# Kernel tuning notes

Measured on AMD Instinct MI355X. Metric: run time of the kernel, lower is better.

## Reference

```python
import jax, jax.numpy as jnp
import numpy as np

ROI_SIZES = (3, 7, 11)
IMAGE_SIZE = 960.0


def setup_inputs() -> dict:
    key = jax.random.key(0)
    ks = jax.random.split(key, 12)
    B, C, H, W = 1, 64, 120, 120
    N = 4096
    feature_maps = jax.random.normal(ks[0], (B, C, H, W), jnp.float32)
    cx = jax.random.uniform(ks[1], (N,), jnp.float32, 100.0, 860.0)
    cy = jax.random.uniform(ks[2], (N,), jnp.float32, 100.0, 860.0)
    bw = jax.random.uniform(ks[3], (N,), jnp.float32, 20.0, 240.0)
    bh = jax.random.uniform(ks[4], (N,), jnp.float32, 20.0, 240.0)
    boxes = jnp.stack([cx - bw / 2, cy - bh / 2, cx + bw / 2, cy + bh / 2], axis=1)
    s = 0.05
    w1 = jax.random.normal(ks[5], (64, 128), jnp.float32) * s
    b1 = jnp.zeros((128,), jnp.float32)
    w2 = jax.random.normal(ks[6], (128, 64), jnp.float32) * s
    b2 = jnp.zeros((64,), jnp.float32)
    p1 = jax.random.normal(ks[7], (256, 128), jnp.float32) * s
    pb1 = jnp.zeros((128,), jnp.float32)
    p2 = jax.random.normal(ks[8], (128, 64), jnp.float32) * s
    pb2 = jnp.zeros((64,), jnp.float32)
    return dict(feature_maps=feature_maps, boxes=boxes, w1=w1, b1=b1, w2=w2, b2=b2,
                p1=p1, pb1=pb1, p2=p2, pb2=pb2)


def _roi_pool(fm0, boxes_norm, r):
    """affine_grid + bilinear grid_sample (align_corners=False, zeros pad) + global avg pool.
    fm0: [C,H,W], boxes_norm: [N,4] in [-1,1]. Returns [N,C]."""
    C, H, W = fm0.shape
    x1, y1, x2, y2 = boxes_norm[:, 0], boxes_norm[:, 1], boxes_norm[:, 2], boxes_norm[:, 3]
    cx = (x1 + x2) / 2
    cy = (y1 + y2) / 2
    bw = jnp.clip(x2 - x1, 1e-6, None)
    bh = jnp.clip(y2 - y1, 1e-6, None)
    # affine_grid base coords with align_corners=False: (2i+1)/r - 1
    lin = (2.0 * jnp.arange(r, dtype=jnp.float32) + 1.0) / r - 1.0
    gx = cx[:, None, None] + (bw / 2)[:, None, None] * lin[None, None, :]  # [N,r,r]
    gy = cy[:, None, None] + (bh / 2)[:, None, None] * lin[None, :, None]  # [N,r,r]
    # normalized -> pixel coords (align_corners=False)
    ix = ((gx + 1.0) * W - 1.0) / 2.0
    iy = ((gy + 1.0) * H - 1.0) / 2.0
    x0f = jnp.floor(ix)
    y0f = jnp.floor(iy)
    wx1 = ix - x0f
    wy1 = iy - y0f
    x0 = x0f.astype(jnp.int32)
    y0 = y0f.astype(jnp.int32)
    fm_flat = fm0.reshape(C, H * W)

    def corner(xi, yi, wt):
        valid = (xi >= 0) & (xi < W) & (yi >= 0) & (yi < H)
        xi_c = jnp.clip(xi, 0, W - 1)
        yi_c = jnp.clip(yi, 0, H - 1)
        idx = yi_c * W + xi_c  # [N,r,r]
        vals = jnp.take(fm_flat, idx.reshape(-1), axis=1).reshape(C, *idx.shape)  # [C,N,r,r]
        return vals * (wt * valid.astype(wt.dtype))[None]

    out = (corner(x0, y0, (1 - wx1) * (1 - wy1))
           + corner(x0 + 1, y0, wx1 * (1 - wy1))
           + corner(x0, y0 + 1, (1 - wx1) * wy1)
           + corner(x0 + 1, y0 + 1, wx1 * wy1))
    return out.mean(axis=(2, 3)).T  # [N,C]


def _shared_head(x, w1, b1, w2, b2):
    h = jax.nn.relu(x @ w1 + b1)
    return jax.nn.relu(h @ w2 + b2)


def reference(feature_maps, boxes, w1, b1, w2, b2, p1, pb1, p2, pb2):
    B, C, H, W = feature_maps.shape
    N = boxes.shape[0]
    boxes_norm = boxes / IMAGE_SIZE * 2.0 - 1.0
    fm0 = feature_maps[0]
    feats = []
    for r in ROI_SIZES:
        pooled = _roi_pool(fm0, boxes_norm, r)  # [N,C]
        feats.append(_shared_head(pooled, w1, b1, w2, b2))
    # global context: avg-pool full map, expand to N
    g = feature_maps.mean(axis=(2, 3))  # [B,C], B=1
    g = jnp.broadcast_to(g, (N, C))
    feats.append(_shared_head(g, w1, b1, w2, b2))
    concat = jnp.concatenate(feats, axis=1)  # [N, 4*64]
    h = jax.nn.relu(concat @ p1 + pb1)
    return jax.nn.relu(h @ p2 + pb2)
```

## Files before the change

kernel.cpp:

```cpp
#include <hip/hip_runtime.h>
#include <hip/hip_bf16.h>


#define HW 120
#define NPIX (HW * HW)

__device__ __forceinline__ float rdlane(float v, int l) {
    return __int_as_float(__builtin_amdgcn_readlane(__float_as_int(v), l));
}

__global__ __launch_bounds__(256) void k_transpose_mean(
    const float* __restrict__ fm, float* __restrict__ fm_t,
    float* __restrict__ partial)
{
    __shared__ float tile[64][65];
    __shared__ float pr[4][64];
    const int t  = threadIdx.x;
    const int tx = t & 63;
    const int ty = t >> 6;
    const int pix0 = blockIdx.x * 64;

    #pragma unroll
    for (int k = 0; k < 16; ++k) {
        const int c = k * 4 + ty;
        tile[c][tx] = fm[c * NPIX + pix0 + tx];
    }
    __syncthreads();
    #pragma unroll
    for (int k = 0; k < 16; ++k) {
        const int p = k * 4 + ty;
        fm_t[(pix0 + p) * 64 + tx] = tile[tx][p];
    }
    float s = 0.f;
    #pragma unroll
    for (int k = 0; k < 16; ++k) s += tile[tx][ty * 16 + k];
    pr[ty][tx] = s;
    __syncthreads();
    if (t < 64)
        partial[blockIdx.x * 64 + t] = pr[0][t] + pr[1][t] + pr[2][t] + pr[3][t];
}

__global__ __launch_bounds__(256) void k_ghead(
    const float* __restrict__ partial,
    const float* __restrict__ w1, const float* __restrict__ b1,
    const float* __restrict__ w2, const float* __restrict__ b2,
    const float* __restrict__ p1, const float* __restrict__ pb1,
    float* __restrict__ f1pre)
{
    __shared__ float pr[4][64];
    __shared__ float g[64];
    __shared__ float h[128];
    __shared__ float gh[64];
    const int t = threadIdx.x;
    const int c = t & 63, q = t >> 6;
    float s = 0.f;
    for (int b = q; b < 225; b += 4) s += partial[b * 64 + c];
    pr[q][c] = s;
    __syncthreads();
    if (t < 64) g[t] = (pr[0][t] + pr[1][t] + pr[2][t] + pr[3][t]) * (1.f / 14400.f);
    __syncthreads();
    if (t < 128) {
        float a = b1[t];
        #pragma unroll 8
        for (int cc = 0; cc < 64; ++cc) a = fmaf(g[cc], w1[cc * 128 + t], a);
        h[t] = fmaxf(a, 0.f);
    }
    __syncthreads();
    if (t < 64) {
        float a = b2[t];
        #pragma unroll 8
        for (int k = 0; k < 128; ++k) a = fmaf(h[k], w2[k * 64 + t], a);
        gh[t] = fmaxf(a, 0.f);
    }
    __syncthreads();
    if (t < 128) {
        float a = pb1[t];
        #pragma unroll 8
        for (int j = 0; j < 64; ++j) a = fmaf(gh[j], p1[(192 + j) * 128 + t], a);
        f1pre[t] = a;
    }
}

__global__ __launch_bounds__(256, 4) void k_fused(
    const float* __restrict__ fm_t, const float* __restrict__ boxes,
    const float* __restrict__ w1, const float* __restrict__ b1,
    const float* __restrict__ w2, const float* __restrict__ b2,
    const float* __restrict__ p1, const float* __restrict__ f1pre,
    const float* __restrict__ p2, const float* __restrict__ pb2,
    float* __restrict__ out, int N)
{
    __shared__ int4   offL[4][192];
    __shared__ float4 wL[4][192];
    const int t    = threadIdx.x;
    const int lane = t & 63;
    const int wid  = t >> 6;
    const int n    = blockIdx.x * 4 + wid;
    if (n >= N) return;

    const float4 bx = reinterpret_cast<const float4*>(boxes)[n];
    const float x1 = bx.x / 960.f * 2.f - 1.f;
    const float y1 = bx.y / 960.f * 2.f - 1.f;
    const float x2 = bx.z / 960.f * 2.f - 1.f;
    const float y2 = bx.w / 960.f * 2.f - 1.f;
    const float cx  = (x1 + x2) * 0.5f;
    const float cy  = (y1 + y2) * 0.5f;
    const float bw2 = fmaxf(x2 - x1, 1e-6f) * 0.5f;
    const float bh2 = fmaxf(y2 - y1, 1e-6f) * 0.5f;

    #pragma unroll
    for (int rep = 0; rep < 3; ++rep) {
        const int p = lane + rep * 64;
        if (p < 179) {
            int i, j; float invR;
            if (p < 9)       { const int lp = p;      invR = 1.f / 3.f;  i = lp / 3;  j = lp - i * 3;  }
            else if (p < 58) { const int lp = p - 9;  invR = 1.f / 7.f;  i = lp / 7;  j = lp - i * 7;  }
            else             { const int lp = p - 58; invR = 1.f / 11.f; i = lp / 11; j = lp - i * 11; }
            const float liny = (float)(2 * i + 1) * invR - 1.f;
            const float linx = (float)(2 * j + 1) * invR - 1.f;
            const float gy = cy + bh2 * liny;
            const float gx = cx + bw2 * linx;
            const float iy = ((gy + 1.f) * 120.f - 1.f) * 0.5f;
            const float ix = ((gx + 1.f) * 120.f - 1.f) * 0.5f;
            const float y0f = floorf(iy), x0f = floorf(ix);
            const float wy = iy - y0f,  wx = ix - x0f;
            const int y0 = (int)y0f, x0 = (int)x0f;
            const float vy0 = (y0 >= 0 && y0 < HW)      ? 1.f : 0.f;
            const float vy1 = (y0 >= -1 && y0 < HW - 1) ? 1.f : 0.f;
            const float vx0 = (x0 >= 0 && x0 < HW)      ? 1.f : 0.f;
            const float vx1 = (x0 >= -1 && x0 < HW - 1) ? 1.f : 0.f;
            const float s2 = invR * invR;
            const int x0c = min(max(x0, 0), HW - 1);
            const int x1c = min(max(x0 + 1, 0), HW - 1);
            const int y0c = min(max(y0, 0), HW - 1);
            const int y1c = min(max(y0 + 1, 0), HW - 1);
            offL[wid][p] = make_int4((y0c * HW + x0c) * 64, (y0c * HW + x1c) * 64,
                                     (y1c * HW + x0c) * 64, (y1c * HW + x1c) * 64);
            wL[wid][p] = make_float4((1.f - wx) * (1.f - wy) * s2 * (vy0 * vx0),
                                     wx * (1.f - wy) * s2 * (vy0 * vx1),
                                     (1.f - wx) * wy * s2 * (vy1 * vx0),
                                     wx * wy * s2 * (vy1 * vx1));
        }
    }

    const float* lb = fm_t + lane;
    float x0s, x1s, x2s;
    {
        float a0, a1, a2, a3;
        #define GATHER(P0, P1, DST)                                        \
        a0 = a1 = a2 = a3 = 0.f;                                           \
        _Pragma("unroll 4")                                                \
        for (int p = (P0); p < (P1); ++p) {                                \
            const int4   o = offL[wid][p];                                 \
            const float4 w = wL[wid][p];                                   \
            a0 = fmaf(w.x, lb[o.x], a0);                                   \
            a1 = fmaf(w.y, lb[o.y], a1);                                   \
            a2 = fmaf(w.z, lb[o.z], a2);                                   \
            a3 = fmaf(w.w, lb[o.w], a3);                                   \
        }                                                                  \
        DST = (a0 + a1) + (a2 + a3);
        GATHER(0, 9, x0s)
        GATHER(9, 58, x1s)
        GATHER(58, 179, x2s)
        #undef GATHER
    }

    float h0l, h0h, h1l, h1h, h2l, h2h;
    {
        const float bl = b1[lane], bh = b1[64 + lane];
        h0l = bl; h0h = bh; h1l = bl; h1h = bh; h2l = bl; h2h = bh;
        #pragma unroll 8
        for (int cc = 0; cc < 64; ++cc) {
            const float wlo = w1[cc * 128 + lane];
            const float whi = w1[cc * 128 + 64 + lane];
            const float xa0 = rdlane(x0s, cc);
            const float xa1 = rdlane(x1s, cc);
            const float xa2 = rdlane(x2s, cc);
            h0l = fmaf(xa0, wlo, h0l); h0h = fmaf(xa0, whi, h0h);
            h1l = fmaf(xa1, wlo, h1l); h1h = fmaf(xa1, whi, h1h);
            h2l = fmaf(xa2, wlo, h2l); h2h = fmaf(xa2, whi, h2h);
        }
        h0l = fmaxf(h0l, 0.f); h0h = fmaxf(h0h, 0.f);
        h1l = fmaxf(h1l, 0.f); h1h = fmaxf(h1h, 0.f);
        h2l = fmaxf(h2l, 0.f); h2h = fmaxf(h2h, 0.f);
    }

    float c0, c1, c2;
    {
        const float bb = b2[lane];
        c0 = bb; c1 = bb; c2 = bb;
        #pragma unroll 8
        for (int cc = 0; cc < 64; ++cc) {
            const float wa = w2[cc * 64 + lane];
            const float wb = w2[(cc + 64) * 64 + lane];
            c0 = fmaf(rdlane(h0l, cc), wa, c0); c0 = fmaf(rdlane(h0h, cc), wb, c0);
            c1 = fmaf(rdlane(h1l, cc), wa, c1); c1 = fmaf(rdlane(h1h, cc), wb, c1);
            c2 = fmaf(rdlane(h2l, cc), wa, c2); c2 = fmaf(rdlane(h2h, cc), wb, c2);
        }
        c0 = fmaxf(c0, 0.f); c1 = fmaxf(c1, 0.f); c2 = fmaxf(c2, 0.f);
    }

    float flo = f1pre[lane], fhi = f1pre[64 + lane];
    {
        #define L3SEG(S, CREG)                                             \
        _Pragma("unroll 8")                                                \
        for (int j = 0; j < 64; ++j) {                                     \
            const int q = (S) * 64 + j;                                    \
            const float wlo = p1[q * 128 + lane];                          \
            const float whi = p1[q * 128 + 64 + lane];                     \
            const float xa = rdlane(CREG, j);                              \
            flo = fmaf(xa, wlo, flo); fhi = fmaf(xa, whi, fhi);            \
        }
        L3SEG(0, c0)
        L3SEG(1, c1)
        L3SEG(2, c2)
        #undef L3SEG
        flo = fmaxf(flo, 0.f); fhi = fmaxf(fhi, 0.f);
    }

    {
        float o = pb2[lane];
        #pragma unroll 8
        for (int j = 0; j < 64; ++j) {
            const float wa = p2[j * 64 + lane];
            const float wb = p2[(j + 64) * 64 + lane];
            o = fmaf(rdlane(flo, j), wa, o);
            o = fmaf(rdlane(fhi, j), wb, o);
        }
        out[n * 64 + lane] = fmaxf(o, 0.f);
    }
}

extern "C" void kernel_launch(void* const* d_in, const int* in_sizes, int n_in,
                              void* d_out, int out_size, void* d_ws, size_t ws_size,
                              hipStream_t stream)
{
    const float* fm    = (const float*)d_in[0];
    const float* boxes = (const float*)d_in[1];
    const float* w1    = (const float*)d_in[2];
    const float* b1    = (const float*)d_in[3];
    const float* w2    = (const float*)d_in[4];
    const float* b2    = (const float*)d_in[5];
    const float* p1    = (const float*)d_in[6];
    const float* pb1   = (const float*)d_in[7];
    const float* p2    = (const float*)d_in[8];
    const float* pb2   = (const float*)d_in[9];
    float* out = (float*)d_out;

    const int N = in_sizes[1] / 4;

    float* ws      = (float*)d_ws;
    float* fm_t    = ws;
    float* partial = fm_t + 921600;
    float* f1pre   = partial + 14400;

    k_transpose_mean<<<NPIX / 64, 256, 0, stream>>>(fm, fm_t, partial);
    k_ghead<<<1, 256, 0, stream>>>(partial, w1, b1, w2, b2, p1, pb1, f1pre);
    k_fused<<<(N + 3) / 4, 256, 0, stream>>>(fm_t, boxes, w1, b1, w2, b2,
                                             p1, f1pre, p2, pb2, out, N);
}
```

Measured before the change: 160.1 us.

## Vectorize ROI gather with float4 channel loads and LDS-broadcast MLP inputs

The bilinear gather now has each lane load a float4 of four channels, with four point groups per wave, and reduces across groups with xor shuffles. This replaces one scalar load per lane per corner. The MLP layers stop using per-element readlane broadcasts. Each layer's activations are written to per-wave LDS buffers and read back as float4 broadcasts. This adds LDS use per block and drops the occupancy hint from launch_bounds, and it relies on implicit wave-level ordering between the LDS writes and reads with no barrier.

New measurement: 150.0 us. 1.07x faster.

```diff
diff --git a/kernel.cpp b/kernel.cpp
--- a/kernel.cpp
+++ b/kernel.cpp
@@ -4,10 +4,6 @@
 
 #define HW 120
 #define NPIX (HW * HW)
-
-__device__ __forceinline__ float rdlane(float v, int l) {
-    return __int_as_float(__builtin_amdgcn_readlane(__float_as_int(v), l));
-}
 
 __global__ __launch_bounds__(256) void k_transpose_mean(
     const float* __restrict__ fm, float* __restrict__ fm_t,
@@ -81,7 +77,35 @@
     }
 }
 
-__global__ __launch_bounds__(256, 4) void k_fused(
+__device__ __forceinline__ float4 gather_seg(
+    const int4* off, const float4* ww, const char* fb, int pg, int P0, int P1)
+{
+    float ax = 0.f, ay = 0.f, az = 0.f, aw = 0.f;
+    #pragma unroll 2
+    for (int p = P0 + pg; p < P1; p += 4) {
+        const int4   o = off[p];
+        const float4 w = ww[p];
+        const float4 v0 = *(const float4*)(fb + o.x);
+        const float4 v1 = *(const float4*)(fb + o.y);
+        const float4 v2 = *(const float4*)(fb + o.z);
+        const float4 v3 = *(const float4*)(fb + o.w);
+        ax = fmaf(w.x, v0.x, ax); ay = fmaf(w.x, v0.y, ay);
+        az = fmaf(w.x, v0.z, az); aw = fmaf(w.x, v0.w, aw);
+        ax = fmaf(w.y, v1.x, ax); ay = fmaf(w.y, v1.y, ay);
+        az = fmaf(w.y, v1.z, az); aw = fmaf(w.y, v1.w, aw);
+        ax = fmaf(w.z, v2.x, ax); ay = fmaf(w.z, v2.y, ay);
+        az = fmaf(w.z, v2.z, az); aw = fmaf(w.z, v2.w, aw);
+        ax = fmaf(w.w, v3.x, ax); ay = fmaf(w.w, v3.y, ay);
+        az = fmaf(w.w, v3.z, az); aw = fmaf(w.w, v3.w, aw);
+    }
+    ax += __shfl_xor(ax, 16, 64); ay += __shfl_xor(ay, 16, 64);
+    az += __shfl_xor(az, 16, 64); aw += __shfl_xor(aw, 16, 64);
+    ax += __shfl_xor(ax, 32, 64); ay += __shfl_xor(ay, 32, 64);
+    az += __shfl_xor(az, 32, 64); aw += __shfl_xor(aw, 32, 64);
+    return make_float4(ax, ay, az, aw);
+}
+
+__global__ __launch_bounds__(256) void k_fused(
     const float* __restrict__ fm_t, const float* __restrict__ boxes,
     const float* __restrict__ w1, const float* __restrict__ b1,
     const float* __restrict__ w2, const float* __restrict__ b2,
@@ -89,13 +113,25 @@
     const float* __restrict__ p2, const float* __restrict__ pb2,
     float* __restrict__ out, int N)
 {
-    __shared__ int4   offL[4][192];
-    __shared__ float4 wL[4][192];
+    __shared__ __align__(16) int4   offS[4][192];
+    __shared__ __align__(16) float4 wS[4][192];
+    __shared__ __align__(16) float  xbufS[4][192];
+    __shared__ __align__(16) float  hbufS[4][384];
+    __shared__ __align__(16) float  cbufS[4][192];
+    __shared__ __align__(16) float  fbufS[4][128];
+
     const int t    = threadIdx.x;
     const int lane = t & 63;
     const int wid  = t >> 6;
     const int n    = blockIdx.x * 4 + wid;
     if (n >= N) return;
+
+    const int4*   off  = offS[wid];
+    const float4* ww   = wS[wid];
+    float* xbuf = xbufS[wid];
+    float* hbuf = hbufS[wid];
+    float* cbuf = cbufS[wid];
+    float* fbuf = fbufS[wid];
 
     const float4 bx = reinterpret_cast<const float4*>(boxes)[n];
     const float x1 = bx.x / 960.f * 2.f - 1.f;
@@ -133,99 +169,112 @@
             const int x1c = min(max(x0 + 1, 0), HW - 1);
             const int y0c = min(max(y0, 0), HW - 1);
             const int y1c = min(max(y0 + 1, 0), HW - 1);
-            offL[wid][p] = make_int4((y0c * HW + x0c) * 64, (y0c * HW + x1c) * 64,
-                                     (y1c * HW + x0c) * 64, (y1c * HW + x1c) * 64);
-            wL[wid][p] = make_float4((1.f - wx) * (1.f - wy) * s2 * (vy0 * vx0),
+            offS[wid][p] = make_int4((y0c * HW + x0c) * 256, (y0c * HW + x1c) * 256,
+                                     (y1c * HW + x0c) * 256, (y1c * HW + x1c) * 256);
+            wS[wid][p] = make_float4((1.f - wx) * (1.f - wy) * s2 * (vy0 * vx0),
                                      wx * (1.f - wy) * s2 * (vy0 * vx1),
                                      (1.f - wx) * wy * s2 * (vy1 * vx0),
                                      wx * wy * s2 * (vy1 * vx1));
         }
     }
 
-    const float* lb = fm_t + lane;
-    float x0s, x1s, x2s;
-    {
-        float a0, a1, a2, a3;
-        #define GATHER(P0, P1, DST)                                        \
-        a0 = a1 = a2 = a3 = 0.f;                                           \
-        _Pragma("unroll 4")                                                \
-        for (int p = (P0); p < (P1); ++p) {                                \
-            const int4   o = offL[wid][p];                                 \
-            const float4 w = wL[wid][p];                                   \
-            a0 = fmaf(w.x, lb[o.x], a0);                                   \
-            a1 = fmaf(w.y, lb[o.y], a1);                                   \
-            a2 = fmaf(w.z, lb[o.z], a2);                                   \
-            a3 = fmaf(w.w, lb[o.w], a3);                                   \
-        }                                                                  \
-        DST = (a0 + a1) + (a2 + a3);
-        GATHER(0, 9, x0s)
-        GATHER(9, 58, x1s)
-        GATHER(58, 179, x2s)
-        #undef GATHER
+    const int qc = lane & 15;
+    const int pg = lane >> 4;
+    const char* fb = (const char*)fm_t + qc * 16;
+
+    const float4 r0 = gather_seg(off, ww, fb, pg, 0, 9);
+    const float4 r1 = gather_seg(off, ww, fb, pg, 9, 58);
+    const float4 r2 = gather_seg(off, ww, fb, pg, 58, 179);
+    if (pg == 0) {
+        *(float4*)(xbuf +       4 * qc) = r0;
+        *(float4*)(xbuf +  64 + 4 * qc) = r1;
+        *(float4*)(xbuf + 128 + 4 * qc) = r2;
     }
 
     float h0l, h0h, h1l, h1h, h2l, h2h;
     {
         const float bl = b1[lane], bh = b1[64 + lane];
-        h0l = bl; h0h = bh; h1l = bl; h1h = bh; h2l = bl; h2h = bh;
-        #pragma unroll 8
-        for (int cc = 0; cc < 64; ++cc) {
-            const float wlo = w1[cc * 128 + lane];
-            const float whi = w1[cc * 128 + 64 + lane];
-            const float xa0 = rdlane(x0s, cc);
-            const float xa1 = rdlane(x1s, cc);
-            const float xa2 = rdlane(x2s, cc);
-            h0l = fmaf(xa0, wlo, h0l); h0h = fmaf(xa0, whi, h0h);
-            h1l = fmaf(xa1, wlo, h1l); h1h = fmaf(xa1, whi, h1h);
-            h2l = fmaf(xa2, wlo, h2l); h2h = fmaf(xa2, whi, h2h);
-        }
+        h0l = h1l = h2l = bl; h0h = h1h = h2h = bh;
+        #define L1STEP(XA0, XA1, XA2, CC) {                                \
+            const float wlo = w1[(CC) * 128 + lane];                       \
+            const float whi = w1[(CC) * 128 + 64 + lane];                  \
+            h0l = fmaf(XA0, wlo, h0l); h0h = fmaf(XA0, whi, h0h);          \
+            h1l = fmaf(XA1, wlo, h1l); h1h = fmaf(XA1, whi, h1h);          \
+            h2l = fmaf(XA2, wlo, h2l); h2h = fmaf(XA2, whi, h2h); }
+        #pragma unroll 4
+        for (int k4 = 0; k4 < 16; ++k4) {
+            const float4 xv0 = *(const float4*)(xbuf +       4 * k4);
+            const float4 xv1 = *(const float4*)(xbuf +  64 + 4 * k4);
+            const float4 xv2 = *(const float4*)(xbuf + 128 + 4 * k4);
+            L1STEP(xv0.x, xv1.x, xv2.x, 4 * k4 + 0)
+            L1STEP(xv0.y, xv1.y, xv2.y, 4 * k4 + 1)
+            L1STEP(xv0.z, xv1.z, xv2.z, 4 * k4 + 2)
+            L1STEP(xv0.w, xv1.w, xv2.w, 4 * k4 + 3)
+        }
+        #undef L1STEP
         h0l = fmaxf(h0l, 0.f); h0h = fmaxf(h0h, 0.f);
         h1l = fmaxf(h1l, 0.f); h1h = fmaxf(h1h, 0.f);
         h2l = fmaxf(h2l, 0.f); h2h = fmaxf(h2h, 0.f);
-    }
-
-    float c0, c1, c2;
+        hbuf[lane]       = h0l; hbuf[64 + lane]  = h0h;
+        hbuf[128 + lane] = h1l; hbuf[192 + lane] = h1h;
+        hbuf[256 + lane] = h2l; hbuf[320 + lane] = h2h;
+    }
+
     {
         const float bb = b2[lane];
-        c0 = bb; c1 = bb; c2 = bb;
-        #pragma unroll 8
-        for (int cc = 0; cc < 64; ++cc) {
-            const float wa = w2[cc * 64 + lane];
-            const float wb = w2[(cc + 64) * 64 + lane];
-            c0 = fmaf(rdlane(h0l, cc), wa, c0); c0 = fmaf(rdlane(h0h, cc), wb, c0);
-            c1 = fmaf(rdlane(h1l, cc), wa, c1); c1 = fmaf(rdlane(h1h, cc), wb, c1);
-            c2 = fmaf(rdlane(h2l, cc), wa, c2); c2 = fmaf(rdlane(h2h, cc), wb, c2);
-        }
-        c0 = fmaxf(c0, 0.f); c1 = fmaxf(c1, 0.f); c2 = fmaxf(c2, 0.f);
-    }
-
-    float flo = f1pre[lane], fhi = f1pre[64 + lane];
+        float c0 = bb, c1 = bb, c2 = bb;
+        #define L2STEP(HA0, HA1, HA2, CC) {                                \
+            const float wa = w2[(CC) * 64 + lane];                         \
+            c0 = fmaf(HA0, wa, c0);                                        \
+            c1 = fmaf(HA1, wa, c1);                                        \
+            c2 = fmaf(HA2, wa, c2); }
+        #pragma unroll 4
+        for (int k4 = 0; k4 < 32; ++k4) {
+            const float4 hv0 = *(const float4*)(hbuf +       4 * k4);
+            const float4 hv1 = *(const float4*)(hbuf + 128 + 4 * k4);
+            const float4 hv2 = *(const float4*)(hbuf + 256 + 4 * k4);
+            L2STEP(hv0.x, hv1.x, hv2.x, 4 * k4 + 0)
+            L2STEP(hv0.y, hv1.y, hv2.y, 4 * k4 + 1)
+            L2STEP(hv0.z, hv1.z, hv2.z, 4 * k4 + 2)
+            L2STEP(hv0.w, hv1.w, hv2.w, 4 * k4 + 3)
+        }
+        #undef L2STEP
+        cbuf[lane]       = fmaxf(c0, 0.f);
+        cbuf[64 + lane]  = fmaxf(c1, 0.f);
+        cbuf[128 + lane] = fmaxf(c2, 0.f);
+    }
+
     {
-        #define L3SEG(S, CREG)                                             \
-        _Pragma("unroll 8")                                                \
-        for (int j = 0; j < 64; ++j) {                                     \
-            const int q = (S) * 64 + j;                                    \
-            const float wlo = p1[q * 128 + lane];                          \
-            const float whi = p1[q * 128 + 64 + lane];                     \
-            const float xa = rdlane(CREG, j);                              \
-            flo = fmaf(xa, wlo, flo); fhi = fmaf(xa, whi, fhi);            \
-        }
-        L3SEG(0, c0)
-        L3SEG(1, c1)
-        L3SEG(2, c2)
-        #undef L3SEG
-        flo = fmaxf(flo, 0.f); fhi = fmaxf(fhi, 0.f);
+        float flo = f1pre[lane], fhi = f1pre[64 + lane];
+        #define L3STEP(CA, QQ) {                                           \
+            const float wlo = p1[(QQ) * 128 + lane];                       \
+            const float whi = p1[(QQ) * 128 + 64 + lane];                  \
+            flo = fmaf(CA, wlo, flo); fhi = fmaf(CA, whi, fhi); }
+        #pragma unroll 4
+        for (int q4 = 0; q4 < 48; ++q4) {
+            const float4 cv = *(const float4*)(cbuf + 4 * q4);
+            L3STEP(cv.x, 4 * q4 + 0)
+            L3STEP(cv.y, 4 * q4 + 1)
+            L3STEP(cv.z, 4 * q4 + 2)
+            L3STEP(cv.w, 4 * q4 + 3)
+        }
+        #undef L3STEP
+        fbuf[lane]      = fmaxf(flo, 0.f);
+        fbuf[64 + lane] = fmaxf(fhi, 0.f);
     }
 
     {
         float o = pb2[lane];
-        #pragma unroll 8
-        for (int j = 0; j < 64; ++j) {
-            const float wa = p2[j * 64 + lane];
-            const float wb = p2[(j + 64) * 64 + lane];
-            o = fmaf(rdlane(flo, j), wa, o);
-            o = fmaf(rdlane(fhi, j), wb, o);
-        }
+        #define L4STEP(FA, JJ) o = fmaf(FA, p2[(JJ) * 64 + lane], o);
+        #pragma unroll 4
+        for (int j4 = 0; j4 < 32; ++j4) {
+            const float4 fv = *(const float4*)(fbuf + 4 * j4);
+            L4STEP(fv.x, 4 * j4 + 0)
+            L4STEP(fv.y, 4 * j4 + 1)
+            L4STEP(fv.z, 4 * j4 + 2)
+            L4STEP(fv.w, 4 * j4 + 3)
+        }
+        #undef L4STEP
         out[n * 64 + lane] = fmaxf(o, 0.f);
     }
 }
```
